# Kernel tuning notes

Measured on AMD Instinct MI355X. Metric: run time of the kernel, lower is better.

## Reference

```python
import jax, jax.numpy as jnp
import numpy as np

N_NODES = 100000
EPS = 1e-5


def _layernorm(x, gamma, beta):
    mu = jnp.mean(x, axis=-1, keepdims=True)
    var = jnp.mean(jnp.square(x - mu), axis=-1, keepdims=True)
    return (x - mu) * jax.lax.rsqrt(var + EPS) * gamma + beta


def _gcn_layer(src, dst, feat, gamma, beta, W, b):
    # copy_u + sum: aggregate source features into destination nodes
    agg = jax.ops.segment_sum(feat[src], dst, num_segments=N_NODES)
    h = _layernorm(agg, gamma, beta)
    return h @ W + b


def setup_inputs() -> dict:
    key = jax.random.key(0)
    ks = jax.random.split(key, 16)
    d_in, d_hid, d_out = 128, 128, 128
    E = 1600000

    def lin(k, fan_in, fan_out):
        kw, kb = jax.random.split(k)
        lim = 1.0 / np.sqrt(fan_in)
        W = jax.random.uniform(kw, (fan_in, fan_out), jnp.float32, -lim, lim)
        b = jax.random.uniform(kb, (fan_out,), jnp.float32, -lim, lim)
        return W, b

    W1, b1 = lin(ks[0], d_in, d_hid)
    W2, b2 = lin(ks[1], d_hid, d_hid)
    W3, b3 = lin(ks[2], d_hid, d_out)
    return {
        "features": jax.random.normal(ks[3], (N_NODES, d_in), jnp.float32),
        "src": jax.random.randint(ks[4], (E,), 0, N_NODES, jnp.int32),
        "dst": jax.random.randint(ks[5], (E,), 0, N_NODES, jnp.int32),
        "g1": jnp.ones((d_in,), jnp.float32), "be1": jnp.zeros((d_in,), jnp.float32),
        "W1": W1, "b1": b1,
        "g2": jnp.ones((d_hid,), jnp.float32), "be2": jnp.zeros((d_hid,), jnp.float32),
        "W2": W2, "b2": b2,
        "g3": jnp.ones((d_hid,), jnp.float32), "be3": jnp.zeros((d_hid,), jnp.float32),
        "W3": W3, "b3": b3,
    }


def reference(features, src, dst, g1, be1, W1, b1, g2, be2, W2, b2, g3, be3, W3, b3):
    x = jax.nn.relu(_gcn_layer(src, dst, features, g1, be1, W1, b1))
    x = jax.nn.relu(_gcn_layer(src, dst, x, g2, be2, W2, b2))
    x = _gcn_layer(src, dst, x, g3, be3, W3, b3)
    return x
```

## Files before the change

### kernel.cpp

```cpp
#include <hip/hip_runtime.h>
#include <hip/hip_bf16.h>
#include <stdint.h>

typedef unsigned short u16;
typedef __attribute__((ext_vector_type(8))) short short8;
typedef __attribute__((ext_vector_type(4))) float f32x4;

#define DIM 128
#define CAP 64
#define LROW 69
#define NB1 512

__device__ __forceinline__ float bflo(uint32_t v) {
    uint32_t b = v << 16;
    float f; __builtin_memcpy(&f, &b, 4); return f;
}
__device__ __forceinline__ float bfhi(uint32_t v) {
    uint32_t b = v & 0xffff0000u;
    float f; __builtin_memcpy(&f, &b, 4); return f;
}
__device__ __forceinline__ u16 f2bf(float f) {
    uint32_t x; __builtin_memcpy(&x, &f, 4);
    uint32_t r = (x + 0x7fffu + ((x >> 16) & 1u)) >> 16;
    return (u16)r;
}
__device__ __forceinline__ uint32_t pack2bf(float a, float b) {
    return (uint32_t)f2bf(a) | ((uint32_t)f2bf(b) << 16);
}


__global__ __launch_bounds__(256) void k_build(
    const int* __restrict__ src, const int* __restrict__ dst,
    uint32_t* __restrict__ gCur, uint32_t* __restrict__ groupBuf,
    int E, int ngrp, int gcap,
    const float* __restrict__ feat, uint32_t* __restrict__ X0,
    uint32_t* __restrict__ X1, uint32_t* __restrict__ X2, int N,
    const float* __restrict__ W1, const float* __restrict__ W2,
    const float* __restrict__ W3,
    u16* __restrict__ t0, u16* __restrict__ t1, u16* __restrict__ t2)
{
    int b = blockIdx.x;
    if (b < NB1) {
        __shared__ uint32_t hcnt[512];
        __shared__ uint32_t hbase[512];
        __shared__ uint32_t hcur[512];
        int per = (E + NB1 - 1) / NB1;
        int lo = b * per;
        int hi = lo + per; if (hi > E) hi = E;

        for (int t = threadIdx.x; t < ngrp; t += 256) { hcnt[t] = 0; hcur[t] = 0; }
        __syncthreads();

        for (int i = lo + threadIdx.x; i < hi; i += 256)
            atomicAdd(&hcnt[((uint32_t)dst[i]) >> 8], 1u);
        __syncthreads();

        int rot = (b * 37) % (ngrp > 0 ? ngrp : 1);
        for (int k = threadIdx.x; k < ngrp; k += 256) {
            int t = k + rot; if (t >= ngrp) t -= ngrp;
            uint32_t c = hcnt[t];
            hbase[t] = c ? atomicAdd(&gCur[t], c) : 0u;
        }
        __syncthreads();

        for (int i = lo + threadIdx.x; i < hi; i += 256) {
            uint32_t d = (uint32_t)dst[i];
            uint32_t g = d >> 8;
            uint32_t off = hbase[g] + atomicAdd(&hcur[g], 1u);
            if (off < (uint32_t)gcap)
                groupBuf[(size_t)g * gcap + off] = (uint32_t)src[i] | ((d & 255u) << 20);
        }
    } else if (b < NB1 + 3) {
        int wi = b - NB1;
        const float* w = wi == 0 ? W1 : (wi == 1 ? W2 : W3);
        u16* o = wi == 0 ? t0 : (wi == 1 ? t1 : t2);
        for (int idx = threadIdx.x; idx < DIM * DIM; idx += blockDim.x) {
            int r = idx >> 7, c = idx & 127;
            o[c * DIM + r] = f2bf(w[idx]);
        }
    } else if (b == NB1 + 3) {
        int t = threadIdx.x;
        if (t < 64)       X0[(size_t)N * 64 + t] = 0u;
        else if (t < 128) X1[(size_t)N * 64 + (t - 64)] = 0u;
        else if (t < 192) X2[(size_t)N * 64 + (t - 128)] = 0u;
    } else {
        int n4 = N * 32;
        int i = (b - (NB1 + 4)) * 256 + threadIdx.x;
        int stride = (gridDim.x - (NB1 + 4)) * 256;
        const float4* in4 = (const float4*)feat;
        uint2* out2 = (uint2*)X0;
        for (; i < n4; i += stride) {
            float4 v = in4[i];
            uint2 r;
            r.x = pack2bf(v.x, v.y);
            r.y = pack2bf(v.z, v.w);
            out2[i] = r;
        }
    }
}


__global__ __launch_bounds__(512) void k_bin2(
    const uint32_t* __restrict__ groupBuf, const uint32_t* __restrict__ gCur,
    uint32_t* __restrict__ bucket, uint32_t* __restrict__ cnt,
    int N, int gcap)
{
    __shared__ uint32_t ncur[256];
    int g = blockIdx.x;
    if (threadIdx.x < 256) ncur[threadIdx.x] = 0;
    __syncthreads();
    uint32_t m = gCur[g]; if (m > (uint32_t)gcap) m = gcap;
    int nodebase = g << 8;
    const uint32_t* buf = groupBuf + (size_t)g * gcap;
    for (uint32_t i = threadIdx.x; i < m; i += 512) {
        uint32_t v = buf[i];
        uint32_t nl = v >> 20;
        uint32_t s = v & 0xFFFFFu;
        uint32_t pos = atomicAdd(&ncur[nl], 1u);
        if (pos < CAP) bucket[(size_t)(nodebase + (int)nl) * CAP + pos] = s;
    }
    __syncthreads();
    int node = nodebase + threadIdx.x;
    if (threadIdx.x < 256 && node < N) cnt[node] = ncur[threadIdx.x];
}


template <int RELU, int OUTF32>
__global__ __launch_bounds__(512) void k_fused(
    const uint32_t* __restrict__ xin, const uint32_t* __restrict__ cnt,
    const uint32_t* __restrict__ bucket,
    const int* __restrict__ src, const int* __restrict__ dst,
    const float* __restrict__ gamma, const float* __restrict__ beta,
    const u16* __restrict__ wt, const float* __restrict__ bias,
    void* __restrict__ outp, int N, int E)
{
    __shared__ uint32_t lds[16 * LROW];
    int w = threadIdx.x >> 6, l = threadIdx.x & 63;
    int base = blockIdx.x * 16;
    int lr = l & 15, lg = l >> 4;

    int col = w * 16 + lr;
    short8 bfrag[4];
#pragma unroll
    for (int kc = 0; kc < 4; ++kc)
        bfrag[kc] = *(const short8*)(wt + (size_t)col * DIM + kc * 32 + lg * 8);
    float bv = bias[col];

    int node0 = __builtin_amdgcn_readfirstlane(base + 2 * w);
    int node1 = node0 + 1;
    int n0c = node0 < N ? node0 : N - 1;
    int n1c = node1 < N ? node1 : N - 1;
    uint32_t c0 = (node0 < N) ? cnt[n0c] : 0u;
    uint32_t c1 = (node1 < N) ? cnt[n1c] : 0u;
    float a0 = 0.f, a1 = 0.f, b0 = 0.f, b1 = 0.f;

    if (__builtin_expect(c0 > CAP || c1 > CAP, 0)) {
        for (int e = 0; e < E; ++e) {
            int d = dst[e];
            if (d == node0) { uint32_t v = xin[(size_t)src[e] * 64 + l]; a0 += bflo(v); a1 += bfhi(v); }
            else if (d == node1) { uint32_t v = xin[(size_t)src[e] * 64 + l]; b0 += bflo(v); b1 += bfhi(v); }
        }
    } else {
        {
            uint32_t bktv = bucket[(size_t)n0c * CAP + l];
#pragma unroll
            for (int g = 0; g < 4; ++g) {
                if ((uint32_t)(g * 16) < c0) {
                    uint32_t v[16];
#pragma unroll
                    for (int i = 0; i < 16; ++i) {
                        const int SLOT = g * 16 + i;
                        uint32_t su = (uint32_t)__builtin_amdgcn_readfirstlane(
                            (int)((uint32_t)__builtin_amdgcn_readlane(bktv, SLOT)));
                        su = ((uint32_t)SLOT < c0) ? su : (uint32_t)N;
                        v[i] = (xin + (size_t)su * 64)[l];
                    }
#pragma unroll
                    for (int i = 0; i < 16; ++i) { a0 += bflo(v[i]); a1 += bfhi(v[i]); }
                }
            }
        }
        {
            uint32_t bktv = bucket[(size_t)n1c * CAP + l];
#pragma unroll
            for (int g = 0; g < 4; ++g) {
                if ((uint32_t)(g * 16) < c1) {
                    uint32_t v[16];
#pragma unroll
                    for (int i = 0; i < 16; ++i) {
                        const int SLOT = g * 16 + i;
                        uint32_t su = (uint32_t)__builtin_amdgcn_readfirstlane(
                            (int)((uint32_t)__builtin_amdgcn_readlane(bktv, SLOT)));
                        su = ((uint32_t)SLOT < c1) ? su : (uint32_t)N;
                        v[i] = (xin + (size_t)su * 64)[l];
                    }
#pragma unroll
                    for (int i = 0; i < 16; ++i) { b0 += bflo(v[i]); b1 += bfhi(v[i]); }
                }
            }
        }
    }

    float sA = a0 + a1, qA = a0 * a0 + a1 * a1;
    float sB = b0 + b1, qB = b0 * b0 + b1 * b1;
    for (int off = 32; off; off >>= 1) {
        sA += __shfl_xor(sA, off, 64);
        sB += __shfl_xor(sB, off, 64);
        qA += __shfl_xor(qA, off, 64);
        qB += __shfl_xor(qB, off, 64);
    }
    float gg0 = gamma[2 * l], gg1 = gamma[2 * l + 1];
    float bb0 = beta[2 * l],  bb1 = beta[2 * l + 1];
    {
        float mean = sA * (1.f / 128.f);
        float var  = qA * (1.f / 128.f) - mean * mean;
        float rs   = rsqrtf(var + 1e-5f);
        lds[(2 * w) * LROW + l] =
            pack2bf((a0 - mean) * rs * gg0 + bb0, (a1 - mean) * rs * gg1 + bb1);
    }
    {
        float mean = sB * (1.f / 128.f);
        float var  = qB * (1.f / 128.f) - mean * mean;
        float rs   = rsqrtf(var + 1e-5f);
        lds[(2 * w + 1) * LROW + l] =
            pack2bf((b0 - mean) * rs * gg0 + bb0, (b1 - mean) * rs * gg1 + bb1);
    }
    __syncthreads();

    const u16* ldsu = (const u16*)lds;
    short8 afrag[4];
#pragma unroll
    for (int kc = 0; kc < 4; ++kc)
        afrag[kc] = *(const short8*)&ldsu[lr * (LROW * 2) + kc * 32 + lg * 8];

    f32x4 acc = {0.f, 0.f, 0.f, 0.f};
#pragma unroll
    for (int kc = 0; kc < 4; ++kc)
        acc = __builtin_amdgcn_mfma_f32_16x16x32_bf16(afrag[kc], bfrag[kc], acc, 0, 0, 0);

#pragma unroll
    for (int j = 0; j < 4; ++j) {
        int row = base + lg * 4 + j;
        float v = acc[j] + bv;
        if (RELU) v = fmaxf(v, 0.f);
        if (row < N) {
            if (OUTF32) ((float*)outp)[(size_t)row * DIM + col] = v;
            else        ((u16*)outp)[(size_t)row * DIM + col] = f2bf(v);
        }
    }
}


extern "C" void kernel_launch(void* const* d_in, const int* in_sizes, int n_in,
                              void* d_out, int out_size, void* d_ws, size_t ws_size,
                              hipStream_t stream) {
    const float* feat = (const float*)d_in[0];
    const int* src  = (const int*)d_in[1];
    const int* dst  = (const int*)d_in[2];
    const float* g1 = (const float*)d_in[3],  *be1 = (const float*)d_in[4];
    const float* W1 = (const float*)d_in[5],  *b1  = (const float*)d_in[6];
    const float* g2 = (const float*)d_in[7],  *be2 = (const float*)d_in[8];
    const float* W2 = (const float*)d_in[9],  *b2  = (const float*)d_in[10];
    const float* g3 = (const float*)d_in[11], *be3 = (const float*)d_in[12];
    const float* W3 = (const float*)d_in[13], *b3  = (const float*)d_in[14];

    int N = in_sizes[0] / DIM;
    int E = in_sizes[1];
    float* out = (float*)d_out;

    int ngrp = (N + 255) >> 8;
    int gcap = (E / (ngrp > 0 ? ngrp : 1)) * 3 / 2 + 1024;

    char* ws = (char*)d_ws;
    auto alloc = [&](size_t bytes) {
        char* p = ws;
        ws += (bytes + 255) & ~(size_t)255;
        return p;
    };
    uint32_t* gCur     = (uint32_t*)alloc((size_t)ngrp * 4);
    uint32_t* groupBuf = (uint32_t*)alloc((size_t)ngrp * gcap * 4);
    uint32_t* cnt      = (uint32_t*)alloc((size_t)N * 4);
    uint32_t* bucket   = (uint32_t*)alloc((size_t)N * CAP * 4);
    u16* wt1 = (u16*)alloc(DIM * DIM * 2);
    u16* wt2 = (u16*)alloc(DIM * DIM * 2);
    u16* wt3 = (u16*)alloc(DIM * DIM * 2);
    uint32_t* X0 = (uint32_t*)alloc((size_t)(N + 1) * 64 * 4);
    uint32_t* X1 = (uint32_t*)alloc((size_t)(N + 1) * 64 * 4);
    uint32_t* X2 = (uint32_t*)alloc((size_t)(N + 1) * 64 * 4);

    hipMemsetAsync(gCur, 0, (size_t)ngrp * 4, stream);
    k_build<<<NB1 + 4 + 1024, 256, 0, stream>>>(src, dst, gCur, groupBuf, E, ngrp, gcap,
                                                feat, X0, X1, X2, N, W1, W2, W3, wt1, wt2, wt3);
    k_bin2<<<ngrp, 512, 0, stream>>>(groupBuf, gCur, bucket, cnt, N, gcap);

    int fblocks = (N + 15) / 16;

    k_fused<1, 0><<<fblocks, 512, 0, stream>>>(X0, cnt, bucket, src, dst, g1, be1, wt1, b1, X1,  N, E);
    k_fused<1, 0><<<fblocks, 512, 0, stream>>>(X1, cnt, bucket, src, dst, g2, be2, wt2, b2, X2,  N, E);
    k_fused<0, 1><<<fblocks, 512, 0, stream>>>(X2, cnt, bucket, src, dst, g3, be3, wt3, b3, out, N, E);
}
```

Measured before the change: 265.1 us.

## Stage bucketed edges in LDS before scattering to group buffers

The edge-bucketing pass now computes a local prefix sum over group counts and places each edge into shared memory in group-sorted order. It then writes those entries out to the global group buffer in a second pass, so consecutive threads write runs of contiguous addresses instead of random ones. The aim is to improve write coalescing of the scatter. The cost is about 30 KB of static LDS per block, which now also applies to the non-build blocks and may lower occupancy, plus the extra scan and sync steps.

```diff
diff --git a/kernel.cpp b/kernel.cpp
--- a/kernel.cpp
+++ b/kernel.cpp
@@ -10,6 +10,7 @@
 #define CAP 64
 #define LROW 69
 #define NB1 512
+#define STAGE 3328
 
 __device__ __forceinline__ float bflo(uint32_t v) {
     uint32_t b = v << 16;
@@ -39,36 +40,73 @@
     const float* __restrict__ W3,
     u16* __restrict__ t0, u16* __restrict__ t1, u16* __restrict__ t2)
 {
+    __shared__ uint32_t hcnt[512];
+    __shared__ uint32_t hbase[512];
+    __shared__ uint32_t lbase[512];
+    __shared__ uint32_t hcur[512];
+    __shared__ uint32_t psum[256];
+    __shared__ uint32_t sval[STAGE];
+    __shared__ uint32_t starg[STAGE];
+
     int b = blockIdx.x;
     if (b < NB1) {
-        __shared__ uint32_t hcnt[512];
-        __shared__ uint32_t hbase[512];
-        __shared__ uint32_t hcur[512];
         int per = (E + NB1 - 1) / NB1;
         int lo = b * per;
         int hi = lo + per; if (hi > E) hi = E;
-
-        for (int t = threadIdx.x; t < ngrp; t += 256) { hcnt[t] = 0; hcur[t] = 0; }
+        int cntE = hi - lo;
+        int t = threadIdx.x;
+
+        for (int k = t; k < 512; k += 256) { hcnt[k] = 0; hcur[k] = 0; }
         __syncthreads();
 
-        for (int i = lo + threadIdx.x; i < hi; i += 256)
+        for (int i = lo + t; i < hi; i += 256)
             atomicAdd(&hcnt[((uint32_t)dst[i]) >> 8], 1u);
         __syncthreads();
 
         int rot = (b * 37) % (ngrp > 0 ? ngrp : 1);
-        for (int k = threadIdx.x; k < ngrp; k += 256) {
-            int t = k + rot; if (t >= ngrp) t -= ngrp;
-            uint32_t c = hcnt[t];
-            hbase[t] = c ? atomicAdd(&gCur[t], c) : 0u;
-        }
+        for (int k = t; k < ngrp; k += 256) {
+            int g = k + rot; if (g >= ngrp) g -= ngrp;
+            uint32_t c = hcnt[g];
+            hbase[g] = c ? atomicAdd(&gCur[g], c) : 0u;
+        }
+        uint32_t ea = hcnt[2 * t], eb = hcnt[2 * t + 1];
+        psum[t] = ea + eb;
         __syncthreads();
-
-        for (int i = lo + threadIdx.x; i < hi; i += 256) {
-            uint32_t d = (uint32_t)dst[i];
-            uint32_t g = d >> 8;
-            uint32_t off = hbase[g] + atomicAdd(&hcur[g], 1u);
-            if (off < (uint32_t)gcap)
-                groupBuf[(size_t)g * gcap + off] = (uint32_t)src[i] | ((d & 255u) << 20);
+        for (int off = 1; off < 256; off <<= 1) {
+            uint32_t u = (t >= off) ? psum[t - off] : 0u;
+            __syncthreads();
+            psum[t] += u;
+            __syncthreads();
+        }
+        uint32_t ex = psum[t] - (ea + eb);
+        lbase[2 * t] = ex;
+        lbase[2 * t + 1] = ex + ea;
+        __syncthreads();
+
+        if (cntE <= STAGE) {
+            for (int i = lo + t; i < hi; i += 256) {
+                uint32_t d = (uint32_t)dst[i];
+                uint32_t g = d >> 8;
+                uint32_t pos = atomicAdd(&hcur[g], 1u);
+                uint32_t li = lbase[g] + pos;
+                uint32_t go = hbase[g] + pos;
+                sval[li] = (uint32_t)src[i] | ((d & 255u) << 20);
+                starg[li] = (go < (uint32_t)gcap)
+                              ? (uint32_t)(g * (uint32_t)gcap + go) : 0xFFFFFFFFu;
+            }
+            __syncthreads();
+            for (int i = t; i < cntE; i += 256) {
+                uint32_t tg = starg[i];
+                if (tg != 0xFFFFFFFFu) groupBuf[tg] = sval[i];
+            }
+        } else {
+            for (int i = lo + t; i < hi; i += 256) {
+                uint32_t d = (uint32_t)dst[i];
+                uint32_t g = d >> 8;
+                uint32_t off = hbase[g] + atomicAdd(&hcur[g], 1u);
+                if (off < (uint32_t)gcap)
+                    groupBuf[(size_t)g * gcap + off] = (uint32_t)src[i] | ((d & 255u) << 20);
+            }
         }
     } else if (b < NB1 + 3) {
         int wi = b - NB1;
```

After: 255.9 us, median of 2. 1.04x faster.
